# Optimization experiments

Hardware: AMD Instinct MI355X
Metric: run time of the kernel (lower is better)

Reference implementation:

```python
import jax, jax.numpy as jnp
import numpy as np

EPS = 1e-5
NUM_HEADS = 4


def setup_inputs() -> dict:
    key = jax.random.key(0)
    ks = jax.random.split(key, 10)
    B, C, H, W = 16, 512, 32, 32
    s = 1.0 / np.sqrt(C)
    x = jax.random.normal(ks[0], (B, C, H, W), dtype=jnp.float32)
    gn_weight = jnp.ones((C,), jnp.float32)
    gn_bias = jnp.zeros((C,), jnp.float32)
    wq = jax.random.uniform(ks[1], (C, C), jnp.float32, -s, s)
    bq = jax.random.uniform(ks[2], (C,), jnp.float32, -s, s)
    wk = jax.random.uniform(ks[3], (C, C), jnp.float32, -s, s)
    bk = jax.random.uniform(ks[4], (C,), jnp.float32, -s, s)
    wv = jax.random.uniform(ks[5], (C, C), jnp.float32, -s, s)
    bv = jax.random.uniform(ks[6], (C,), jnp.float32, -s, s)
    wo = jax.random.uniform(ks[7], (C, C), jnp.float32, -s, s)
    bo = jax.random.uniform(ks[8], (C,), jnp.float32, -s, s)
    return dict(x=x, gn_weight=gn_weight, gn_bias=gn_bias, wq=wq, bq=bq,
                wk=wk, bk=bk, wv=wv, bv=bv, wo=wo, bo=bo)


def reference(x, gn_weight, gn_bias, wq, bq, wk, bk, wv, bv, wo, bo):
    B, C, H, W = x.shape
    head_size = C // NUM_HEADS

    # GroupNorm(num_groups=1): normalize over (C,H,W) per batch element
    mean = jnp.mean(x, axis=(1, 2, 3), keepdims=True)
    var = jnp.var(x, axis=(1, 2, 3), keepdims=True)
    xn = (x - mean) / jnp.sqrt(var + EPS)
    xn = xn * gn_weight[None, :, None, None] + gn_bias[None, :, None, None]

    # (B, C, H, W) -> (B, S, C) with S = H*W
    seq = xn.reshape(B, C, H * W).transpose(0, 2, 1)

    def heads(y):  # (B, S, C) -> (B, nh, S, hd)
        return y.reshape(B, H * W, NUM_HEADS, head_size).transpose(0, 2, 1, 3)

    q = heads(seq @ wq.T + bq)
    k = heads(seq @ wk.T + bk)
    v = heads(seq @ wv.T + bv)

    scores = jnp.einsum('bhqd,bhkd->bhqk', q, k) / np.sqrt(head_size).astype(np.float32)
    attn = jax.nn.softmax(scores, axis=-1)
    out = jnp.einsum('bhqk,bhkd->bhqd', attn, v)  # (B, nh, S, hd)

    out = out.transpose(0, 2, 1, 3).reshape(B, H * W, C)
    out = out @ wo.T + bo
    out = out.transpose(0, 2, 1).reshape(B, C, H, W)
    return out + x
```

## Files before the change

### kernel.cpp

```cpp
#include <hip/hip_runtime.h>
#include <stdint.h>

#define B_  16
#define C_  512
#define S_  1024
#define NH  4
#define HD  128
#define BS  (B_*S_)

typedef __attribute__((ext_vector_type(8))) short   short8;
typedef __attribute__((ext_vector_type(4))) float   f32x4;
typedef __attribute__((ext_vector_type(4))) unsigned int uint4v;

__device__ __forceinline__ unsigned short f2bf(float f) {
    unsigned u = __float_as_uint(f);
    unsigned r = (u + 0x7fffu + ((u >> 16) & 1u)) >> 16;
    return (unsigned short)r;
}

__device__ __forceinline__ unsigned cvt_pk_bf16(float a, float b) {
    unsigned r;
    asm("v_cvt_pk_bf16_f32 %0, %1, %2" : "=v"(r) : "v"(a), "v"(b));
    return r;
}

__global__ void gn_partial(const float* __restrict__ x, float* __restrict__ part) {
    int b = blockIdx.x, chunk = blockIdx.y;
    const float4* xb = (const float4*)(x + (size_t)b * C_ * S_);
    int base = chunk * 4096 + threadIdx.x;
    float s = 0.f, ss = 0.f;
#pragma unroll
    for (int i = 0; i < 16; ++i) {
        float4 v = xb[base + i * 256];
        s  += v.x + v.y + v.z + v.w;
        ss += v.x*v.x + v.y*v.y + v.z*v.z + v.w*v.w;
    }
    for (int off = 32; off; off >>= 1) { s += __shfl_down(s, off); ss += __shfl_down(ss, off); }
    __shared__ float red[2][4];
    int wv = threadIdx.x >> 6;
    if ((threadIdx.x & 63) == 0) { red[0][wv] = s; red[1][wv] = ss; }
    __syncthreads();
    if (threadIdx.x == 0) {
        s  = red[0][0] + red[0][1] + red[0][2] + red[0][3];
        ss = red[1][0] + red[1][1] + red[1][2] + red[1][3];
        part[(b*32 + chunk)*2 + 0] = s;
        part[(b*32 + chunk)*2 + 1] = ss;
    }
}

__global__ void gn_apply_t(const float* __restrict__ x, const float* __restrict__ part,
                           const float* __restrict__ gw, const float* __restrict__ gb,
                           unsigned short* __restrict__ seq) {
    int st = blockIdx.x, ct = blockIdx.y, b = blockIdx.z;
    float s1 = 0.f, s2 = 0.f;
#pragma unroll
    for (int i = 0; i < 32; ++i) { s1 += part[(b*32+i)*2]; s2 += part[(b*32+i)*2+1]; }
    const float invN = 1.0f / (float)(C_ * S_);
    float mean = s1 * invN;
    float var  = s2 * invN - mean * mean;
    float rstd = rsqrtf(var + 1e-5f);

    __shared__ unsigned short tile[64][72];
    int c0 = ct * 64, s0 = st * 64;
    const float* xb = x + ((size_t)b * C_ + c0) * S_ + s0;
    int tr = threadIdx.x >> 4, tj = (threadIdx.x & 15) * 4;
#pragma unroll
    for (int p = 0; p < 4; ++p) {
        int i = tr + p * 16;
        float w  = gw[c0 + i];
        float bb = gb[c0 + i];
        float4 v = *(const float4*)(xb + (size_t)i * S_ + tj);
        tile[i][tj+0] = f2bf((v.x - mean) * rstd * w + bb);
        tile[i][tj+1] = f2bf((v.y - mean) * rstd * w + bb);
        tile[i][tj+2] = f2bf((v.z - mean) * rstd * w + bb);
        tile[i][tj+3] = f2bf((v.w - mean) * rstd * w + bb);
    }
    __syncthreads();
    int j  = threadIdx.x >> 2;
    int cc = (threadIdx.x & 3) * 16;
    unsigned short tmp[16] __attribute__((aligned(16)));
#pragma unroll
    for (int i = 0; i < 16; ++i) tmp[i] = tile[cc + i][j];
    unsigned short* dst = seq + ((size_t)(b * S_ + s0 + j)) * C_ + c0 + cc;
    *(uint4v*)dst       = *(uint4v*)tmp;
    *(uint4v*)(dst + 8) = *(uint4v*)(tmp + 8);
}

__global__ void cvt_w(const float* __restrict__ wq, const float* __restrict__ wk,
                      const float* __restrict__ wv, const float* __restrict__ wo,
                      unsigned short* __restrict__ wqkv, unsigned short* __restrict__ wobf) {
    int m = blockIdx.y;
    const float* src = (m == 0) ? wq : (m == 1) ? wk : (m == 2) ? wv : wo;
    unsigned short* dst = (m < 3) ? (wqkv + (size_t)m * C_ * C_) : wobf;
    int i = blockIdx.x * 256 + threadIdx.x;
    float4 v = ((const float4*)src)[i];
    unsigned short o[4] __attribute__((aligned(8)));
    o[0] = f2bf(v.x); o[1] = f2bf(v.y); o[2] = f2bf(v.z); o[3] = f2bf(v.w);
    *(unsigned long long*)(dst + (size_t)i * 4) = *(unsigned long long*)o;
}

__device__ __forceinline__ void gemm128_bt(const unsigned short* __restrict__ Ab,
                                           const unsigned short* __restrict__ Bb,
                                           const int K,
                                           unsigned short* lA, unsigned short* lB,
                                           f32x4 acc[4][4]) {
    const int t = threadIdx.x;
    const int w = t >> 6, l = t & 63;
    const int wr = (w >> 1) * 64, wc = (w & 1) * 64;
    const int lrow = l & 15;
    const int lk8  = (l >> 4) * 8;
#pragma unroll
    for (int mi = 0; mi < 4; ++mi)
#pragma unroll
        for (int ni = 0; ni < 4; ++ni)
            acc[mi][ni] = (f32x4){0.f, 0.f, 0.f, 0.f};

    for (int kt = 0; kt < K; kt += 64) {
#pragma unroll
        for (int j = 0; j < 4; ++j) {
            const int lin = j * 256 + t;
            const int row = lin >> 3, ch = lin & 7;
            __builtin_amdgcn_global_load_lds(
                (const __attribute__((address_space(1))) unsigned int*)(Ab + (size_t)row * K + kt + ch * 8),
                (__attribute__((address_space(3))) unsigned int*)(lA + (size_t)(j * 256 + w * 64) * 8),
                16, 0, 0);
        }
#pragma unroll
        for (int j = 0; j < 4; ++j) {
            const int lin = j * 256 + t;
            const int row = lin >> 3, ch = lin & 7;
            __builtin_amdgcn_global_load_lds(
                (const __attribute__((address_space(1))) unsigned int*)(Bb + (size_t)row * K + kt + ch * 8),
                (__attribute__((address_space(3))) unsigned int*)(lB + (size_t)(j * 256 + w * 64) * 8),
                16, 0, 0);
        }
        __syncthreads();
#pragma unroll
        for (int kk = 0; kk < 2; ++kk) {
            short8 af[4], bf[4];
            const int ko = lk8 + kk * 32;
#pragma unroll
            for (int mi = 0; mi < 4; ++mi)
                af[mi] = *(const short8*)&lA[(size_t)(wr + mi * 16 + lrow) * 64 + ko];
#pragma unroll
            for (int ni = 0; ni < 4; ++ni)
                bf[ni] = *(const short8*)&lB[(size_t)(wc + ni * 16 + lrow) * 64 + ko];
#pragma unroll
            for (int mi = 0; mi < 4; ++mi)
#pragma unroll
                for (int ni = 0; ni < 4; ++ni)
                    acc[mi][ni] = __builtin_amdgcn_mfma_f32_16x16x32_bf16(af[mi], bf[ni], acc[mi][ni], 0, 0, 0);
        }
        __syncthreads();
    }
}

__global__ __launch_bounds__(256) void qkv_gemm(
        const unsigned short* __restrict__ seq, const unsigned short* __restrict__ wqkv,
        const float* __restrict__ bq, const float* __restrict__ bk, const float* __restrict__ bv,
        unsigned short* __restrict__ qb, unsigned short* __restrict__ kb, unsigned short* __restrict__ vtb) {
    __shared__ unsigned short sbuf[128 * 136];
    unsigned short* lA = sbuf;
    unsigned short* lB = sbuf + 128 * 64;
    int mb = blockIdx.x, nb = blockIdx.y;
    f32x4 acc[4][4];
    gemm128_bt(seq + (size_t)mb * 128 * C_, wqkv + (size_t)nb * 128 * C_, C_, lA, lB, acc);

    int mat = nb >> 2;
    int cb = (nb & 3) * 128;
    int w = threadIdx.x >> 6, l = threadIdx.x & 63;
    int l15 = l & 15, g = l >> 4;
    int wr = (w >> 1) * 64, wc = (w & 1) * 64;

    if (mat < 2) {
        const float* bias = (mat == 0) ? bq : bk;
        unsigned short* out = (mat == 0) ? qb : kb;
        float oscale = (mat == 0) ? 0.12751879523087253f : 1.0f;
#pragma unroll
        for (int mi = 0; mi < 4; ++mi)
#pragma unroll
            for (int ni = 0; ni < 4; ++ni)
#pragma unroll
                for (int r = 0; r < 4; ++r) {
                    int m = mb * 128 + wr + mi * 16 + g * 4 + r;
                    int c = cb + wc + ni * 16 + l15;
                    int b = m >> 10, s = m & 1023;
                    int h = c >> 7,  d = c & 127;
                    float v = (acc[mi][ni][r] + bias[c]) * oscale;
                    out[(((size_t)(b * NH + h) * S_) + s) * HD + d] = f2bf(v);
                }
    } else {
        int b  = mb >> 3;
        int s0 = (mb & 7) * 128;
        int h  = nb & 3;
#pragma unroll
        for (int mi = 0; mi < 4; ++mi)
#pragma unroll
            for (int ni = 0; ni < 4; ++ni) {
                int dloc = wc + ni * 16 + l15;
                int mloc = wr + mi * 16 + g * 4;
                float bia = bv[h * 128 + dloc];
#pragma unroll
                for (int r = 0; r < 4; ++r)
                    sbuf[dloc * 136 + mloc + r] = f2bf(acc[mi][ni][r] + bia);
            }
        __syncthreads();
        unsigned short* dst = vtb + ((size_t)(b * NH + h)) * HD * S_ + s0;
#pragma unroll
        for (int p = 0; p < 8; ++p) {
            int idx = p * 256 + threadIdx.x;
            int d = idx >> 4, cc = (idx & 15) * 8;
            short8 vv = *(const short8*)&sbuf[d * 136 + cc];
            *(short8*)(dst + (size_t)d * S_ + cc) = vv;
        }
    }
}

__global__ __launch_bounds__(256) void flash_attn(
        const unsigned short* __restrict__ q, const unsigned short* __restrict__ k,
        const unsigned short* __restrict__ vt, unsigned short* __restrict__ o) {
    int bh = blockIdx.x, qblk = blockIdx.y;
    int t = threadIdx.x, w = t >> 6, l = t & 63;
    int l15 = l & 15, g = l >> 4;
    int swz = (l15 & 7) << 1;
    __shared__ unsigned short lK[2][64 * 128];
    __shared__ unsigned short lV[2][128 * 64];
    __shared__ unsigned short lP[4][32 * 64];

    const size_t bh_base = (size_t)bh * S_ * HD;
    int q0 = qblk * 128 + w * 32;

    short8 qa[4], qb_[4];
    const unsigned short* qp = q + bh_base + (size_t)(q0 + l15) * HD + g * 8;
#pragma unroll
    for (int kc = 0; kc < 4; ++kc) {
        qa[kc]  = *(const short8*)(qp + kc * 32);
        qb_[kc] = *(const short8*)(qp + 16 * HD + kc * 32);
    }

    f32x4 oa[8], ob[8];
#pragma unroll
    for (int i = 0; i < 8; ++i) { oa[i] = (f32x4){0.f,0.f,0.f,0.f}; ob[i] = (f32x4){0.f,0.f,0.f,0.f}; }
    float m_a = -1e30f, l_a = 0.f, m_b = -1e30f, l_b = 0.f;
    unsigned short* myP = &lP[w][0];

#define STAGE_TILE(buf, kv0_) do {                                                     \
    int kv0s = (kv0_);                                                                 \
    _Pragma("unroll")                                                                  \
    for (int j = 0; j < 4; ++j) {                                                      \
        int lin = j * 256 + t;                                                         \
        int row = lin >> 4, c16 = lin & 15;                                            \
        int sc  = (c16 & 8) | ((c16 ^ row) & 7);                                       \
        __builtin_amdgcn_global_load_lds(                                              \
            (const __attribute__((address_space(1))) unsigned int*)(k + bh_base + (size_t)(kv0s + row) * HD + sc * 8), \
            (__attribute__((address_space(3))) unsigned int*)(&lK[buf][0] + (size_t)(j * 256 + w * 64) * 8), \
            16, 0, 0);                                                                 \
    }                                                                                  \
    _Pragma("unroll")                                                                  \
    for (int j = 0; j < 4; ++j) {                                                      \
        int lin = j * 256 + t;                                                         \
        int row = lin >> 3, c8 = lin & 7;                                              \
        int sc  = (c8 ^ row) & 7;                                                      \
        __builtin_amdgcn_global_load_lds(                                              \
            (const __attribute__((address_space(1))) unsigned int*)(vt + bh_base + (size_t)row * S_ + kv0s + sc * 8), \
            (__attribute__((address_space(3))) unsigned int*)(&lV[buf][0] + (size_t)(j * 256 + w * 64) * 8), \
            16, 0, 0);                                                                 \
    }                                                                                  \
} while (0)

    STAGE_TILE(0, 0);
    __syncthreads();
    int cur = 0;

    for (int kt = 0; kt < 16; ++kt) {
        if (kt < 15) STAGE_TILE(cur ^ 1, (kt + 1) * 64);
        const unsigned short* lKc = &lK[cur][0];
        const unsigned short* lVc = &lV[cur][0];

        f32x4 sa[4], sb[4];
#pragma unroll
        for (int nb = 0; nb < 4; ++nb) {
            sa[nb] = (f32x4){0.f,0.f,0.f,0.f};
            sb[nb] = (f32x4){0.f,0.f,0.f,0.f};
        }
#pragma unroll
        for (int kc = 0; kc < 4; ++kc)
#pragma unroll
            for (int nb = 0; nb < 4; ++nb) {
                int row = nb * 16 + l15;
                int gg  = g + kc * 4;
                int ch  = (gg & 8) | ((gg ^ row) & 7);
                short8 kf = *(const short8*)&lKc[(size_t)row * 128 + ch * 8];
                sa[nb] = __builtin_amdgcn_mfma_f32_16x16x32_bf16(kf, qa[kc],  sa[nb], 0, 0, 0);
                sb[nb] = __builtin_amdgcn_mfma_f32_16x16x32_bf16(kf, qb_[kc], sb[nb], 0, 0, 0);
            }

        float mxa = fmaxf(fmaxf(sa[0][0], sa[0][1]), fmaxf(sa[0][2], sa[0][3]));
        float mxb = fmaxf(fmaxf(sb[0][0], sb[0][1]), fmaxf(sb[0][2], sb[0][3]));
#pragma unroll
        for (int nb = 1; nb < 4; ++nb) {
            mxa = fmaxf(mxa, fmaxf(fmaxf(sa[nb][0], sa[nb][1]), fmaxf(sa[nb][2], sa[nb][3])));
            mxb = fmaxf(mxb, fmaxf(fmaxf(sb[nb][0], sb[nb][1]), fmaxf(sb[nb][2], sb[nb][3])));
        }
        mxa = fmaxf(mxa, __shfl_xor(mxa, 16)); mxa = fmaxf(mxa, __shfl_xor(mxa, 32));
        mxb = fmaxf(mxb, __shfl_xor(mxb, 16)); mxb = fmaxf(mxb, __shfl_xor(mxb, 32));

        if (!__all((mxa - m_a <= 8.f) && (mxb - m_b <= 8.f))) {
            float mna = fmaxf(m_a, mxa), mnb = fmaxf(m_b, mxb);
            float ala = exp2f(m_a - mna), alb = exp2f(m_b - mnb);
            m_a = mna; m_b = mnb; l_a *= ala; l_b *= alb;
            float a0 = __shfl(ala, g*4+0), a1 = __shfl(ala, g*4+1),
                  a2 = __shfl(ala, g*4+2), a3 = __shfl(ala, g*4+3);
            float b0 = __shfl(alb, g*4+0), b1 = __shfl(alb, g*4+1),
                  b2 = __shfl(alb, g*4+2), b3 = __shfl(alb, g*4+3);
#pragma unroll
            for (int dn = 0; dn < 8; ++dn) {
                oa[dn][0] *= a0; oa[dn][1] *= a1; oa[dn][2] *= a2; oa[dn][3] *= a3;
                ob[dn][0] *= b0; ob[dn][1] *= b1; ob[dn][2] *= b2; ob[dn][3] *= b3;
            }
        }

        float psa = 0.f, psb = 0.f;
#pragma unroll
        for (int nb = 0; nb < 4; ++nb) {
            float p0 = exp2f(sa[nb][0] - m_a), p1 = exp2f(sa[nb][1] - m_a);
            float p2 = exp2f(sa[nb][2] - m_a), p3 = exp2f(sa[nb][3] - m_a);
            psa += (p0 + p1) + (p2 + p3);
            unsigned d0 = cvt_pk_bf16(p0, p1), d1 = cvt_pk_bf16(p2, p3);
            int c = (nb * 4 + g) ^ swz;
            *(unsigned long long*)(myP + l15 * 64 + c * 4) =
                (unsigned long long)d0 | ((unsigned long long)d1 << 32);
            float r0 = exp2f(sb[nb][0] - m_b), r1 = exp2f(sb[nb][1] - m_b);
            float r2 = exp2f(sb[nb][2] - m_b), r3 = exp2f(sb[nb][3] - m_b);
            psb += (r0 + r1) + (r2 + r3);
            unsigned e0 = cvt_pk_bf16(r0, r1), e1 = cvt_pk_bf16(r2, r3);
            *(unsigned long long*)(myP + (l15 + 16) * 64 + c * 4) =
                (unsigned long long)e0 | ((unsigned long long)e1 << 32);
        }
        psa += __shfl_xor(psa, 16); psa += __shfl_xor(psa, 32);
        psb += __shfl_xor(psb, 16); psb += __shfl_xor(psb, 32);
        l_a += psa; l_b += psb;

#pragma unroll
        for (int kc = 0; kc < 2; ++kc) {
            int c0 = (kc * 8 + g * 2) ^ swz;
            short8 pa = *(const short8*)(myP + l15 * 64 + c0 * 4);
            short8 pb = *(const short8*)(myP + (l15 + 16) * 64 + c0 * 4);
            int pg = g + kc * 4;
#pragma unroll
            for (int dn = 0; dn < 8; ++dn) {
                int vrow = dn * 16 + l15;
                int vch  = (pg ^ vrow) & 7;
                short8 vf = *(const short8*)&lVc[(size_t)vrow * 64 + vch * 8];
                oa[dn] = __builtin_amdgcn_mfma_f32_16x16x32_bf16(pa, vf, oa[dn], 0, 0, 0);
                ob[dn] = __builtin_amdgcn_mfma_f32_16x16x32_bf16(pb, vf, ob[dn], 0, 0, 0);
            }
        }
        __syncthreads();
        cur ^= 1;
    }
#undef STAGE_TILE

    float ia = 1.0f / l_a, ib = 1.0f / l_b;
    float ia0 = __shfl(ia, g*4+0), ia1 = __shfl(ia, g*4+1),
          ia2 = __shfl(ia, g*4+2), ia3 = __shfl(ia, g*4+3);
    float ib0 = __shfl(ib, g*4+0), ib1 = __shfl(ib, g*4+1),
          ib2 = __shfl(ib, g*4+2), ib3 = __shfl(ib, g*4+3);
    int b = bh >> 2, h = bh & 3;
    int sra = q0 + g * 4;
#pragma unroll
    for (int dn = 0; dn < 8; ++dn) {
        int cbase = h * HD + dn * 16 + l15;
        o[((size_t)(b * S_ + sra + 0)) * C_ + cbase]  = f2bf(oa[dn][0] * ia0);
        o[((size_t)(b * S_ + sra + 1)) * C_ + cbase]  = f2bf(oa[dn][1] * ia1);
        o[((size_t)(b * S_ + sra + 2)) * C_ + cbase]  = f2bf(oa[dn][2] * ia2);
        o[((size_t)(b * S_ + sra + 3)) * C_ + cbase]  = f2bf(oa[dn][3] * ia3);
        o[((size_t)(b * S_ + sra + 16)) * C_ + cbase] = f2bf(ob[dn][0] * ib0);
        o[((size_t)(b * S_ + sra + 17)) * C_ + cbase] = f2bf(ob[dn][1] * ib1);
        o[((size_t)(b * S_ + sra + 18)) * C_ + cbase] = f2bf(ob[dn][2] * ib2);
        o[((size_t)(b * S_ + sra + 19)) * C_ + cbase] = f2bf(ob[dn][3] * ib3);
    }
}

__global__ __launch_bounds__(256) void oproj_gemm(
        const unsigned short* __restrict__ wobf, const unsigned short* __restrict__ attn,
        const float* __restrict__ bo, const float* __restrict__ x, float* __restrict__ out) {
    int cbk = blockIdx.x, sb = blockIdx.y, b = blockIdx.z;
    __shared__ unsigned short lA[128 * 64], lB[128 * 64];
    f32x4 acc[4][4];
    gemm128_bt(wobf + (size_t)cbk * 128 * C_,
               attn + ((size_t)b * S_ + sb * 128) * C_, C_, lA, lB, acc);

    int w = threadIdx.x >> 6, l = threadIdx.x & 63;
    int wr = (w >> 1) * 64, wc = (w & 1) * 64;
#pragma unroll
    for (int mi = 0; mi < 4; ++mi)
#pragma unroll
        for (int ni = 0; ni < 4; ++ni)
#pragma unroll
            for (int r = 0; r < 4; ++r) {
                int c = cbk * 128 + wr + mi * 16 + (l >> 4) * 4 + r;
                int s = sb * 128 + wc + ni * 16 + (l & 15);
                size_t off = ((size_t)b * C_ + c) * S_ + s;
                out[off] = acc[mi][ni][r] + bo[c] + x[off];
            }
}

extern "C" void kernel_launch(void* const* d_in, const int* in_sizes, int n_in,
                              void* d_out, int out_size, void* d_ws, size_t ws_size,
                              hipStream_t stream) {
    const float* x  = (const float*)d_in[0];
    const float* gw = (const float*)d_in[1];
    const float* gb = (const float*)d_in[2];
    const float* wq = (const float*)d_in[3];
    const float* bq = (const float*)d_in[4];
    const float* wk = (const float*)d_in[5];
    const float* bk = (const float*)d_in[6];
    const float* wv = (const float*)d_in[7];
    const float* bv = (const float*)d_in[8];
    const float* wo = (const float*)d_in[9];
    const float* bo = (const float*)d_in[10];
    float* out = (float*)d_out;

    char* ws = (char*)d_ws;
    const size_t SEQ_BYTES = (size_t)BS * C_ * 2;
    float* part           = (float*)ws;
    unsigned short* seq   = (unsigned short*)(ws + 4096);
    unsigned short* wqkv  = (unsigned short*)(ws + 4096 + SEQ_BYTES);
    unsigned short* wobf  = (unsigned short*)(ws + 4096 + SEQ_BYTES + 1572864);
    unsigned short* qb    = (unsigned short*)(ws + 4096 + SEQ_BYTES + 1572864 + 524288);
    unsigned short* kb    = qb + 8388608;
    unsigned short* vtb   = kb + 8388608;
    unsigned short* attn  = seq;

    gn_partial<<<dim3(16, 32), 256, 0, stream>>>(x, part);
    gn_apply_t<<<dim3(16, 8, 16), 256, 0, stream>>>(x, part, gw, gb, seq);
    cvt_w<<<dim3(256, 4), 256, 0, stream>>>(wq, wk, wv, wo, wqkv, wobf);
    qkv_gemm<<<dim3(128, 12), 256, 0, stream>>>(seq, wqkv, bq, bk, bv, qb, kb, vtb);
    flash_attn<<<dim3(64, 8), 256, 0, stream>>>(qb, kb, vtb, attn);
    oproj_gemm<<<dim3(4, 8, 16), 256, 0, stream>>>(wobf, attn, bo, x, out);
}
```

Baseline: 147.2 us.

## Halve flash-attention KV tile to raise occupancy, precompute LDS offsets, add setprio

Shrinks the flash-attention KV tile from 64 to 32 keys, which halves shared memory for K, V and P and doubles the number of loop iterations. It requests 4 blocks per CU through launch_bounds, precomputes the swizzled LDS offsets for K, V and P outside the loop, and wraps the MFMA sections in s_setprio. The aim is more resident waves to hide latency, at the cost of twice as many barriers and softmax-rescale steps per query block.

```diff
diff --git a/kernel.cpp b/kernel.cpp
--- a/kernel.cpp
+++ b/kernel.cpp
@@ -216,16 +216,15 @@
     }
 }
 
-__global__ __launch_bounds__(256) void flash_attn(
+__global__ __launch_bounds__(256, 4) void flash_attn(
         const unsigned short* __restrict__ q, const unsigned short* __restrict__ k,
         const unsigned short* __restrict__ vt, unsigned short* __restrict__ o) {
     int bh = blockIdx.x, qblk = blockIdx.y;
     int t = threadIdx.x, w = t >> 6, l = t & 63;
     int l15 = l & 15, g = l >> 4;
-    int swz = (l15 & 7) << 1;
-    __shared__ unsigned short lK[2][64 * 128];
-    __shared__ unsigned short lV[2][128 * 64];
-    __shared__ unsigned short lP[4][32 * 64];
+    __shared__ unsigned short lK[2][32 * 128];
+    __shared__ unsigned short lV[2][128 * 32];
+    __shared__ unsigned short lP[4][32 * 32];
 
     const size_t bh_base = (size_t)bh * S_ * HD;
     int q0 = qblk * 128 + w * 32;
@@ -238,6 +237,27 @@
         qb_[kc] = *(const short8*)(qp + 16 * HD + kc * 32);
     }
 
+    int koffs[4][2];
+#pragma unroll
+    for (int kc = 0; kc < 4; ++kc)
+#pragma unroll
+        for (int nb = 0; nb < 2; ++nb) {
+            int row = nb * 16 + l15, gg = g + kc * 4;
+            int ch  = (gg & 8) | ((gg ^ row) & 7);
+            koffs[kc][nb] = row * 128 + ch * 8;
+        }
+    int voffs[8];
+#pragma unroll
+    for (int dn = 0; dn < 8; ++dn) {
+        int row = dn * 16 + l15;
+        voffs[dn] = row * 32 + ((g ^ row) & 3) * 8;
+    }
+    int sw  = l15 & 7;
+    int pw0 = l15 * 32 + ((g)     ^ sw) * 4;
+    int pw1 = l15 * 32 + ((4 + g) ^ sw) * 4;
+    int pr0 = l15 * 32 + ((2*g)     ^ sw) * 4;
+    int pr1 = l15 * 32 + ((2*g + 1) ^ sw) * 4;
+
     f32x4 oa[8], ob[8];
 #pragma unroll
     for (int i = 0; i < 8; ++i) { oa[i] = (f32x4){0.f,0.f,0.f,0.f}; ob[i] = (f32x4){0.f,0.f,0.f,0.f}; }
@@ -247,7 +267,7 @@
 #define STAGE_TILE(buf, kv0_) do {                                                     \
     int kv0s = (kv0_);                                                                 \
     _Pragma("unroll")                                                                  \
-    for (int j = 0; j < 4; ++j) {                                                      \
+    for (int j = 0; j < 2; ++j) {                                                      \
         int lin = j * 256 + t;                                                         \
         int row = lin >> 4, c16 = lin & 15;                                            \
         int sc  = (c16 & 8) | ((c16 ^ row) & 7);                                       \
@@ -257,10 +277,10 @@
             16, 0, 0);                                                                 \
     }                                                                                  \
     _Pragma("unroll")                                                                  \
-    for (int j = 0; j < 4; ++j) {                                                      \
+    for (int j = 0; j < 2; ++j) {                                                      \
         int lin = j * 256 + t;                                                         \
-        int row = lin >> 3, c8 = lin & 7;                                              \
-        int sc  = (c8 ^ row) & 7;                                                      \
+        int row = lin >> 2, c4 = lin & 3;                                              \
+        int sc  = (c4 ^ row) & 3;                                                      \
         __builtin_amdgcn_global_load_lds(                                              \
             (const __attribute__((address_space(1))) unsigned int*)(vt + bh_base + (size_t)row * S_ + kv0s + sc * 8), \
             (__attribute__((address_space(3))) unsigned int*)(&lV[buf][0] + (size_t)(j * 256 + w * 64) * 8), \
@@ -272,36 +292,32 @@
     __syncthreads();
     int cur = 0;
 
-    for (int kt = 0; kt < 16; ++kt) {
-        if (kt < 15) STAGE_TILE(cur ^ 1, (kt + 1) * 64);
+    for (int kt = 0; kt < 32; ++kt) {
+        if (kt < 31) STAGE_TILE(cur ^ 1, (kt + 1) * 32);
         const unsigned short* lKc = &lK[cur][0];
         const unsigned short* lVc = &lV[cur][0];
 
-        f32x4 sa[4], sb[4];
-#pragma unroll
-        for (int nb = 0; nb < 4; ++nb) {
+        f32x4 sa[2], sb[2];
+#pragma unroll
+        for (int nb = 0; nb < 2; ++nb) {
             sa[nb] = (f32x4){0.f,0.f,0.f,0.f};
             sb[nb] = (f32x4){0.f,0.f,0.f,0.f};
         }
+        __builtin_amdgcn_s_setprio(1);
 #pragma unroll
         for (int kc = 0; kc < 4; ++kc)
 #pragma unroll
-            for (int nb = 0; nb < 4; ++nb) {
-                int row = nb * 16 + l15;
-                int gg  = g + kc * 4;
-                int ch  = (gg & 8) | ((gg ^ row) & 7);
-                short8 kf = *(const short8*)&lKc[(size_t)row * 128 + ch * 8];
+            for (int nb = 0; nb < 2; ++nb) {
+                short8 kf = *(const short8*)&lKc[koffs[kc][nb]];
                 sa[nb] = __builtin_amdgcn_mfma_f32_16x16x32_bf16(kf, qa[kc],  sa[nb], 0, 0, 0);
                 sb[nb] = __builtin_amdgcn_mfma_f32_16x16x32_bf16(kf, qb_[kc], sb[nb], 0, 0, 0);
             }
+        __builtin_amdgcn_s_setprio(0);
 
         float mxa = fmaxf(fmaxf(sa[0][0], sa[0][1]), fmaxf(sa[0][2], sa[0][3]));
         float mxb = fmaxf(fmaxf(sb[0][0], sb[0][1]), fmaxf(sb[0][2], sb[0][3]));
-#pragma unroll
-        for (int nb = 1; nb < 4; ++nb) {
-            mxa = fmaxf(mxa, fmaxf(fmaxf(sa[nb][0], sa[nb][1]), fmaxf(sa[nb][2], sa[nb][3])));
-            mxb = fmaxf(mxb, fmaxf(fmaxf(sb[nb][0], sb[nb][1]), fmaxf(sb[nb][2], sb[nb][3])));
-        }
+        mxa = fmaxf(mxa, fmaxf(fmaxf(sa[1][0], sa[1][1]), fmaxf(sa[1][2], sa[1][3])));
+        mxb = fmaxf(mxb, fmaxf(fmaxf(sb[1][0], sb[1][1]), fmaxf(sb[1][2], sb[1][3])));
         mxa = fmaxf(mxa, __shfl_xor(mxa, 16)); mxa = fmaxf(mxa, __shfl_xor(mxa, 32));
         mxb = fmaxf(mxb, __shfl_xor(mxb, 16)); mxb = fmaxf(mxb, __shfl_xor(mxb, 32));
 
@@ -322,40 +338,37 @@
 
         float psa = 0.f, psb = 0.f;
 #pragma unroll
-        for (int nb = 0; nb < 4; ++nb) {
+        for (int nb = 0; nb < 2; ++nb) {
             float p0 = exp2f(sa[nb][0] - m_a), p1 = exp2f(sa[nb][1] - m_a);
             float p2 = exp2f(sa[nb][2] - m_a), p3 = exp2f(sa[nb][3] - m_a);
             psa += (p0 + p1) + (p2 + p3);
             unsigned d0 = cvt_pk_bf16(p0, p1), d1 = cvt_pk_bf16(p2, p3);
-            int c = (nb * 4 + g) ^ swz;
-            *(unsigned long long*)(myP + l15 * 64 + c * 4) =
+            *(unsigned long long*)(myP + (nb ? pw1 : pw0)) =
                 (unsigned long long)d0 | ((unsigned long long)d1 << 32);
             float r0 = exp2f(sb[nb][0] - m_b), r1 = exp2f(sb[nb][1] - m_b);
             float r2 = exp2f(sb[nb][2] - m_b), r3 = exp2f(sb[nb][3] - m_b);
             psb += (r0 + r1) + (r2 + r3);
             unsigned e0 = cvt_pk_bf16(r0, r1), e1 = cvt_pk_bf16(r2, r3);
-            *(unsigned long long*)(myP + (l15 + 16) * 64 + c * 4) =
+            *(unsigned long long*)(myP + (nb ? pw1 : pw0) + 16 * 32) =
                 (unsigned long long)e0 | ((unsigned long long)e1 << 32);
         }
         psa += __shfl_xor(psa, 16); psa += __shfl_xor(psa, 32);
         psb += __shfl_xor(psb, 16); psb += __shfl_xor(psb, 32);
         l_a += psa; l_b += psb;
 
-#pragma unroll
-        for (int kc = 0; kc < 2; ++kc) {
-            int c0 = (kc * 8 + g * 2) ^ swz;
-            short8 pa = *(const short8*)(myP + l15 * 64 + c0 * 4);
-            short8 pb = *(const short8*)(myP + (l15 + 16) * 64 + c0 * 4);
-            int pg = g + kc * 4;
-#pragma unroll
-            for (int dn = 0; dn < 8; ++dn) {
-                int vrow = dn * 16 + l15;
-                int vch  = (pg ^ vrow) & 7;
-                short8 vf = *(const short8*)&lVc[(size_t)vrow * 64 + vch * 8];
-                oa[dn] = __builtin_amdgcn_mfma_f32_16x16x32_bf16(pa, vf, oa[dn], 0, 0, 0);
-                ob[dn] = __builtin_amdgcn_mfma_f32_16x16x32_bf16(pb, vf, ob[dn], 0, 0, 0);
-            }
-        }
+        union { unsigned long long u[2]; short8 v; } pa, pb;
+        pa.u[0] = *(const unsigned long long*)(myP + pr0);
+        pa.u[1] = *(const unsigned long long*)(myP + pr1);
+        pb.u[0] = *(const unsigned long long*)(myP + pr0 + 16 * 32);
+        pb.u[1] = *(const unsigned long long*)(myP + pr1 + 16 * 32);
+        __builtin_amdgcn_s_setprio(1);
+#pragma unroll
+        for (int dn = 0; dn < 8; ++dn) {
+            short8 vf = *(const short8*)&lVc[voffs[dn]];
+            oa[dn] = __builtin_amdgcn_mfma_f32_16x16x32_bf16(pa.v, vf, oa[dn], 0, 0, 0);
+            ob[dn] = __builtin_amdgcn_mfma_f32_16x16x32_bf16(pb.v, vf, ob[dn], 0, 0, 0);
+        }
+        __builtin_amdgcn_s_setprio(0);
         __syncthreads();
         cur ^= 1;
     }
```

Result: slower. 201.7 us (+37.0%).

## Compute softmax row sums with MFMA against ones and precompute LDS offsets

Applied to the files above, without the earlier changes.

Replaces the per-tile softmax denominator sum (VALU adds plus cross-lane shuffles) with an extra MFMA multiplying the bf16 P tile by a ones vector, so the sum lands in the same layout as the output accumulator. It also precomputes swizzled LDS byte offsets for K, V and P outside the loop so inner loads use simple XOR addressing. It wraps the MFMA phases in s_setprio to favor matrix issue. The row sum is now taken from the bf16-rounded probabilities, which matches the values used in PV, and costs two extra MFMAs per kc step.

```diff
diff --git a/kernel.cpp b/kernel.cpp
--- a/kernel.cpp
+++ b/kernel.cpp
@@ -238,11 +238,34 @@
         qb_[kc] = *(const short8*)(qp + 16 * HD + kc * 32);
     }
 
+    short8 onesf;
+#pragma unroll
+    for (int i = 0; i < 8; ++i) onesf[i] = (short)0x3F80;
+
+    int ko[4];
+#pragma unroll
+    for (int nb = 0; nb < 4; ++nb) {
+        int row = nb * 16 + l15;
+        ko[nb] = row * 256 + ((g ^ row) & 7) * 16;
+    }
+    int vo[8];
+#pragma unroll
+    for (int dn = 0; dn < 8; ++dn) {
+        int row = dn * 16 + l15;
+        vo[dn] = row * 128 + ((g ^ row) & 7) * 16;
+    }
+    int pw[4], pr[2];
+#pragma unroll
+    for (int nb = 0; nb < 4; ++nb) pw[nb] = l15 * 128 + (((nb * 4 + g) ^ swz) * 8);
+#pragma unroll
+    for (int kc = 0; kc < 2; ++kc) pr[kc] = l15 * 128 + (((kc * 8 + g * 2) ^ swz) * 8);
+
     f32x4 oa[8], ob[8];
 #pragma unroll
     for (int i = 0; i < 8; ++i) { oa[i] = (f32x4){0.f,0.f,0.f,0.f}; ob[i] = (f32x4){0.f,0.f,0.f,0.f}; }
-    float m_a = -1e30f, l_a = 0.f, m_b = -1e30f, l_b = 0.f;
-    unsigned short* myP = &lP[w][0];
+    f32x4 lacc_a = (f32x4){0.f,0.f,0.f,0.f}, lacc_b = (f32x4){0.f,0.f,0.f,0.f};
+    float m_a = -1e30f, m_b = -1e30f;
+    char* myP = (char*)&lP[w][0];
 
 #define STAGE_TILE(buf, kv0_) do {                                                     \
     int kv0s = (kv0_);                                                                 \
@@ -274,8 +297,8 @@
 
     for (int kt = 0; kt < 16; ++kt) {
         if (kt < 15) STAGE_TILE(cur ^ 1, (kt + 1) * 64);
-        const unsigned short* lKc = &lK[cur][0];
-        const unsigned short* lVc = &lV[cur][0];
+        const char* lKc = (const char*)&lK[cur][0];
+        const char* lVc = (const char*)&lV[cur][0];
 
         f32x4 sa[4], sb[4];
 #pragma unroll
@@ -283,17 +306,16 @@
             sa[nb] = (f32x4){0.f,0.f,0.f,0.f};
             sb[nb] = (f32x4){0.f,0.f,0.f,0.f};
         }
+        __builtin_amdgcn_s_setprio(1);
 #pragma unroll
         for (int kc = 0; kc < 4; ++kc)
 #pragma unroll
             for (int nb = 0; nb < 4; ++nb) {
-                int row = nb * 16 + l15;
-                int gg  = g + kc * 4;
-                int ch  = (gg & 8) | ((gg ^ row) & 7);
-                short8 kf = *(const short8*)&lKc[(size_t)row * 128 + ch * 8];
+                short8 kf = *(const short8*)(lKc + (ko[nb] ^ (kc << 6)));
                 sa[nb] = __builtin_amdgcn_mfma_f32_16x16x32_bf16(kf, qa[kc],  sa[nb], 0, 0, 0);
                 sb[nb] = __builtin_amdgcn_mfma_f32_16x16x32_bf16(kf, qb_[kc], sb[nb], 0, 0, 0);
             }
+        __builtin_amdgcn_s_setprio(0);
 
         float mxa = fmaxf(fmaxf(sa[0][0], sa[0][1]), fmaxf(sa[0][2], sa[0][3]));
         float mxb = fmaxf(fmaxf(sb[0][0], sb[0][1]), fmaxf(sb[0][2], sb[0][3]));
@@ -308,11 +330,13 @@
         if (!__all((mxa - m_a <= 8.f) && (mxb - m_b <= 8.f))) {
             float mna = fmaxf(m_a, mxa), mnb = fmaxf(m_b, mxb);
             float ala = exp2f(m_a - mna), alb = exp2f(m_b - mnb);
-            m_a = mna; m_b = mnb; l_a *= ala; l_b *= alb;
+            m_a = mna; m_b = mnb;
             float a0 = __shfl(ala, g*4+0), a1 = __shfl(ala, g*4+1),
                   a2 = __shfl(ala, g*4+2), a3 = __shfl(ala, g*4+3);
             float b0 = __shfl(alb, g*4+0), b1 = __shfl(alb, g*4+1),
                   b2 = __shfl(alb, g*4+2), b3 = __shfl(alb, g*4+3);
+            lacc_a[0] *= a0; lacc_a[1] *= a1; lacc_a[2] *= a2; lacc_a[3] *= a3;
+            lacc_b[0] *= b0; lacc_b[1] *= b1; lacc_b[2] *= b2; lacc_b[3] *= b3;
 #pragma unroll
             for (int dn = 0; dn < 8; ++dn) {
                 oa[dn][0] *= a0; oa[dn][1] *= a1; oa[dn][2] *= a2; oa[dn][3] *= a3;
@@ -320,52 +344,44 @@
             }
         }
 
-        float psa = 0.f, psb = 0.f;
 #pragma unroll
         for (int nb = 0; nb < 4; ++nb) {
             float p0 = exp2f(sa[nb][0] - m_a), p1 = exp2f(sa[nb][1] - m_a);
             float p2 = exp2f(sa[nb][2] - m_a), p3 = exp2f(sa[nb][3] - m_a);
-            psa += (p0 + p1) + (p2 + p3);
             unsigned d0 = cvt_pk_bf16(p0, p1), d1 = cvt_pk_bf16(p2, p3);
-            int c = (nb * 4 + g) ^ swz;
-            *(unsigned long long*)(myP + l15 * 64 + c * 4) =
+            *(unsigned long long*)(myP + pw[nb]) =
                 (unsigned long long)d0 | ((unsigned long long)d1 << 32);
             float r0 = exp2f(sb[nb][0] - m_b), r1 = exp2f(sb[nb][1] - m_b);
             float r2 = exp2f(sb[nb][2] - m_b), r3 = exp2f(sb[nb][3] - m_b);
-            psb += (r0 + r1) + (r2 + r3);
             unsigned e0 = cvt_pk_bf16(r0, r1), e1 = cvt_pk_bf16(r2, r3);
-            *(unsigned long long*)(myP + (l15 + 16) * 64 + c * 4) =
+            *(unsigned long long*)(myP + pw[nb] + 2048) =
                 (unsigned long long)e0 | ((unsigned long long)e1 << 32);
         }
-        psa += __shfl_xor(psa, 16); psa += __shfl_xor(psa, 32);
-        psb += __shfl_xor(psb, 16); psb += __shfl_xor(psb, 32);
-        l_a += psa; l_b += psb;
-
+
+        __builtin_amdgcn_s_setprio(1);
 #pragma unroll
         for (int kc = 0; kc < 2; ++kc) {
-            int c0 = (kc * 8 + g * 2) ^ swz;
-            short8 pa = *(const short8*)(myP + l15 * 64 + c0 * 4);
-            short8 pb = *(const short8*)(myP + (l15 + 16) * 64 + c0 * 4);
-            int pg = g + kc * 4;
+            short8 pa = *(const short8*)(myP + pr[kc]);
+            short8 pb = *(const short8*)(myP + pr[kc] + 2048);
+            lacc_a = __builtin_amdgcn_mfma_f32_16x16x32_bf16(pa, onesf, lacc_a, 0, 0, 0);
+            lacc_b = __builtin_amdgcn_mfma_f32_16x16x32_bf16(pb, onesf, lacc_b, 0, 0, 0);
 #pragma unroll
             for (int dn = 0; dn < 8; ++dn) {
-                int vrow = dn * 16 + l15;
-                int vch  = (pg ^ vrow) & 7;
-                short8 vf = *(const short8*)&lVc[(size_t)vrow * 64 + vch * 8];
+                short8 vf = *(const short8*)(lVc + (vo[dn] ^ (kc << 6)));
                 oa[dn] = __builtin_amdgcn_mfma_f32_16x16x32_bf16(pa, vf, oa[dn], 0, 0, 0);
                 ob[dn] = __builtin_amdgcn_mfma_f32_16x16x32_bf16(pb, vf, ob[dn], 0, 0, 0);
             }
         }
+        __builtin_amdgcn_s_setprio(0);
         __syncthreads();
         cur ^= 1;
     }
 #undef STAGE_TILE
 
-    float ia = 1.0f / l_a, ib = 1.0f / l_b;
-    float ia0 = __shfl(ia, g*4+0), ia1 = __shfl(ia, g*4+1),
-          ia2 = __shfl(ia, g*4+2), ia3 = __shfl(ia, g*4+3);
-    float ib0 = __shfl(ib, g*4+0), ib1 = __shfl(ib, g*4+1),
-          ib2 = __shfl(ib, g*4+2), ib3 = __shfl(ib, g*4+3);
+    float ia0 = 1.0f / lacc_a[0], ia1 = 1.0f / lacc_a[1],
+          ia2 = 1.0f / lacc_a[2], ia3 = 1.0f / lacc_a[3];
+    float ib0 = 1.0f / lacc_b[0], ib1 = 1.0f / lacc_b[1],
+          ib2 = 1.0f / lacc_b[2], ib3 = 1.0f / lacc_b[3];
     int b = bh >> 2, h = bh & 3;
     int sra = q0 + g * 4;
 #pragma unroll
```

After: 173.8 us. 18.1% more time.
